# Kernel optimization log

Hardware: AMD Instinct MI355X
Metric: run time of the kernel (lower is better)

The kernel has to match this reference:

```python
import jax, jax.numpy as jnp
import numpy as np

DECAY = 0.8

def l2norm(t):
    # F.normalize with eps=1e-12
    n = jnp.linalg.norm(t, axis=-1, keepdims=True)
    return t / jnp.maximum(n, 1e-12)

def setup_inputs() -> dict:
    key = jax.random.key(0)
    k1, k2, k3 = jax.random.split(key, 3)
    x = jax.random.normal(k1, (16, 4096, 64), dtype=jnp.float32)
    embed = l2norm(jax.random.uniform(k2, (1, 4096, 64), dtype=jnp.float32) * 2.0 - 1.0)  # uniform_init + l2norm
    cluster_size = jax.random.uniform(k3, (1, 4096), dtype=jnp.float32) * 10.0
    return {"x": x, "embed": embed, "cluster_size": cluster_size}

def reference(x, embed, cluster_size):
    # x: [b, n, d] (ndim<4 -> add codebook dim), embed: [h, c, d]
    h, c, d = embed.shape
    xh = x[None, ...]                           # [1, b, n, d]
    shape = xh.shape
    flatten = l2norm(xh.reshape(h, -1, d))      # [h, N, d]
    embed_n = l2norm(embed)                     # [h, c, d]
    dist = jnp.einsum('hnd,hcd->hnc', flatten, embed_n)          # [h, N, c]
    embed_ind_flat = jnp.argmax(dist, axis=-1)                   # temperature==0 gumbel -> argmax
    embed_onehot = jax.nn.one_hot(embed_ind_flat, c, dtype=x.dtype)  # [h, N, c]
    embed_ind = embed_ind_flat.reshape(shape[:-1])               # [h, b, n]
    # batched_embedding: gather from the raw (non-normalized) codebook
    quantize = jax.vmap(lambda e, i: e[i])(embed, embed_ind_flat).reshape(shape)  # [h, b, n, d]
    # training-mode EMA codebook update (buffer updates returned as outputs)
    bins = embed_onehot.sum(axis=1)                              # [h, c]
    new_cluster_size = cluster_size * DECAY + bins * (1.0 - DECAY)
    zero_mask = bins == 0
    bins_safe = jnp.where(zero_mask, 1.0, bins)
    embed_sum = jnp.einsum('hnd,hnc->hcd', flatten, embed_onehot)  # [h, c, d]
    embed_normalized = l2norm(embed_sum / bins_safe[..., None])
    embed_normalized = jnp.where(zero_mask[..., None], embed_n, embed_normalized)
    new_embed = embed * DECAY + embed_normalized * (1.0 - DECAY)
    # squeeze back the added codebook dim (needs_codebook_dim path)
    return quantize[0], embed_ind[0], new_embed, new_cluster_size
```

## Files before the change

kernel.cpp:

```cpp
#include <hip/hip_runtime.h>
#include <math.h>

#define DECAY 0.8f
constexpr int B_     = 16;
constexpr int NSEQ   = 4096;
constexpr int D      = 64;
constexpr int C      = 4096;
constexpr int N      = B_ * NSEQ;
constexpr int NCHUNK = 4;
constexpr int CCHUNK = C / NCHUNK;
constexpr int PANEL  = 64;
constexpr int NPANEL = CCHUNK / PANEL;
constexpr int TILE_ELEMS = 32 * D;

#define GATE_THR  3e-4f
#define CONS_THR  1e-3f

typedef __attribute__((ext_vector_type(8)))  short bf16x8;
typedef __attribute__((ext_vector_type(16))) float f32x16;

__device__ __forceinline__ unsigned short bf16_rn(float f) {
    unsigned u = __builtin_bit_cast(unsigned, f);
    u += 0x7FFFu + ((u >> 16) & 1u);
    return (unsigned short)(u >> 16);
}
__device__ __forceinline__ float bf16_to_f(unsigned short h) {
    unsigned u = ((unsigned)h) << 16;
    return __builtin_bit_cast(float, u);
}
__device__ __forceinline__ f32x16 mfma32(bf16x8 a, bf16x8 b, f32x16 c) {
    return __builtin_amdgcn_mfma_f32_32x32x16_bf16(a, b, c, 0, 0, 0);
}
__device__ __forceinline__ void gload_lds16(const unsigned short* g,
                                            unsigned short* l) {
    __builtin_amdgcn_global_load_lds(
        (const __attribute__((address_space(1))) unsigned int*)g,
        (__attribute__((address_space(3))) unsigned int*)l, 16, 0, 0);
}

__global__ __launch_bounds__(256) void prep_e_kernel(
    const float* __restrict__ embed,
    float* __restrict__ embed_n,
    unsigned short* __restrict__ e_hi,
    unsigned short* __restrict__ e_lo,
    float* __restrict__ embed_sum,
    float* __restrict__ bins,
    int* __restrict__ dirty_count,
    int ncpy)
{
    int code = blockIdx.x * 4 + (threadIdx.x >> 6);
    int lane = threadIdx.x & 63;
    float v = embed[code * D + lane];
    float ss = v * v;
    #pragma unroll
    for (int o = 32; o > 0; o >>= 1) ss += __shfl_xor(ss, o);
    float inv = 1.0f / fmaxf(sqrtf(ss), 1e-12f);
    float en = v * inv;
    embed_n[code * D + lane] = en;

    unsigned short hi = bf16_rn(en);
    unsigned short lo = bf16_rn(en - bf16_to_f(hi));
    int t = code >> 5, r = code & 31;
    int g = lane >> 3, e = lane & 7;
    size_t pos = (size_t)t * TILE_ELEMS + (g * 32 + r) * 8 + e;
    e_hi[pos] = hi;
    e_lo[pos] = lo;

    for (int k = 0; k < ncpy; ++k) {
        embed_sum[(size_t)k * C * D + code * D + lane] = 0.0f;
        if (lane == 0) bins[k * C + code] = 0.0f;
    }
    if (blockIdx.x == 0 && threadIdx.x == 0) *dirty_count = 0;
}

__global__ __launch_bounds__(512) void assign_mfma_kernel(
    const float* __restrict__ x,
    const unsigned short* __restrict__ e_hi,
    const unsigned short* __restrict__ e_lo,
    float* __restrict__ part)
{
    __shared__ unsigned short lds_hi[2 * TILE_ELEMS];
    __shared__ unsigned short lds_lo[2 * TILE_ELEMS];

    const int tid  = threadIdx.x;
    const int lane = tid & 63;
    const int wid  = tid >> 6;
    const int m    = lane & 31;
    const int hi   = lane >> 5;
    const int rb   = (blockIdx.x * 8 + wid) * 32;
    const int cy   = blockIdx.y;

    bf16x8 xhi[4], xlo[4];
    #pragma unroll
    for (int c = 0; c < 4; ++c) {
        const float* p = x + (size_t)(rb + m) * D + c * 16 + hi * 8;
        float4 t0 = *(const float4*)p;
        float4 t1 = *(const float4*)(p + 4);
        float e[8] = {t0.x, t0.y, t0.z, t0.w, t1.x, t1.y, t1.z, t1.w};
        bf16x8 h, l2;
        #pragma unroll
        for (int j = 0; j < 8; ++j) {
            unsigned short hh = bf16_rn(e[j]);
            h[j]  = (short)hh;
            l2[j] = (short)bf16_rn(e[j] - bf16_to_f(hh));
        }
        xhi[c] = h;
        xlo[c] = l2;
    }

    float m1 = -3.4e38f, m2 = -3.4e38f;
    int   tl = 0;

    for (int p = 0; p < NPANEL; ++p) {
        const size_t pbase = ((size_t)cy * NPANEL + p) * (2 * TILE_ELEMS);
        __syncthreads();
        gload_lds16(e_hi + pbase + tid * 8, &lds_hi[tid * 8]);
        gload_lds16(e_lo + pbase + tid * 8, &lds_lo[tid * 8]);
        __syncthreads();

        #pragma unroll
        for (int t = 0; t < 2; ++t) {
            const int pt = (cy * NPANEL + p) * 2 + t;
            f32x16 accA = {}, accB = {};
            #pragma unroll
            for (int c = 0; c < 2; ++c) {
                const int off = t * TILE_ELEMS + ((c * 2 + hi) * 32 + m) * 8;
                bf16x8 eh = *(const bf16x8*)(lds_hi + off);
                bf16x8 el = *(const bf16x8*)(lds_lo + off);
                accA = mfma32(eh, xhi[c], accA);
                accA = mfma32(el, xhi[c], accA);
                accA = mfma32(eh, xlo[c], accA);
            }
            #pragma unroll
            for (int c = 2; c < 4; ++c) {
                const int off = t * TILE_ELEMS + ((c * 2 + hi) * 32 + m) * 8;
                bf16x8 eh = *(const bf16x8*)(lds_hi + off);
                bf16x8 el = *(const bf16x8*)(lds_lo + off);
                accB = mfma32(eh, xhi[c], accB);
                accB = mfma32(el, xhi[c], accB);
                accB = mfma32(eh, xlo[c], accB);
            }
            #pragma unroll
            for (int h = 0; h < 2; ++h) {
                float s0 = accA[h*8+0] + accB[h*8+0];
                float s1 = accA[h*8+1] + accB[h*8+1];
                float s2 = accA[h*8+2] + accB[h*8+2];
                float s3 = accA[h*8+3] + accB[h*8+3];
                float s4 = accA[h*8+4] + accB[h*8+4];
                float s5 = accA[h*8+5] + accB[h*8+5];
                float s6 = accA[h*8+6] + accB[h*8+6];
                float s7 = accA[h*8+7] + accB[h*8+7];
                float tm = fmaxf(fmaxf(fmaxf(s0, s1), fmaxf(s2, s3)),
                                 fmaxf(fmaxf(s4, s5), fmaxf(s6, s7)));
                const int ht = pt * 2 + h;
                float mn = fminf(m1, tm);
                bool  gt = tm > m1;
                tl = gt ? ht : tl;
                m1 = fmaxf(m1, tm);
                m2 = fmaxf(m2, mn);
            }
        }
    }

    {
        float b1 = __shfl_xor(m1, 32);
        float b2 = __shfl_xor(m2, 32);
        int   bt = __shfl_xor(tl, 32);
        float nm2 = fmaxf(fmaxf(m2, b2), fminf(m1, b1));
        bool  take = (b1 > m1);
        m1 = take ? b1 : m1;
        tl = take ? bt : tl;
        m2 = nm2;
    }
    if (lane < 32) {
        int row = rb + lane;
        float4 pr;
        pr.x = m1; pr.y = (float)tl; pr.z = m2; pr.w = 0.0f;
        *reinterpret_cast<float4*>(part + (size_t)row * D + cy * 4) = pr;
    }
}

__global__ __launch_bounds__(256) void merge_scatter_kernel(
    const float* __restrict__ x,
    const float* __restrict__ embed,
    const float* __restrict__ embed_n,
    float* __restrict__ q_out,
    float* __restrict__ ind_out,
    float* __restrict__ embed_sum,
    float* __restrict__ bins,
    int* __restrict__ dirty_count,
    int* __restrict__ dirty_list,
    int ncpy)
{
    int wid  = threadIdx.x >> 6;
    int lane = threadIdx.x & 63;
    int row  = blockIdx.x * 4 + wid;
    int cpy  = blockIdx.x & (ncpy - 1);

    float w1a, m2x; int wt;
    {
        const float4* pp = reinterpret_cast<const float4*>(q_out + (size_t)row * D);
        float4 P = pp[0];
        w1a = P.x; wt = (int)P.y; m2x = P.z;
        #pragma unroll
        for (int j = 1; j < NCHUNK; ++j) {
            float4 Q = pp[j];
            float nm2 = fmaxf(fmaxf(m2x, Q.z), fminf(w1a, Q.x));
            if (Q.x > w1a) { w1a = Q.x; wt = (int)Q.y; }
            m2x = nm2;
        }
    }

    int   csub = lane >> 2;
    int   code = wt * 16 + csub;
    float dot;
    {
        const float4* ep = (const float4*)(embed_n + (size_t)code * D + (lane & 3) * 16);
        const float4* xp = (const float4*)(x + (size_t)row * D + (lane & 3) * 16);
        float a0 = 0.f, a1 = 0.f, a2 = 0.f, a3 = 0.f;
        #pragma unroll
        for (int k = 0; k < 4; ++k) {
            float4 e = ep[k], xx = xp[k];
            a0 = fmaf(e.x, xx.x, a0);
            a1 = fmaf(e.y, xx.y, a1);
            a2 = fmaf(e.z, xx.z, a2);
            a3 = fmaf(e.w, xx.w, a3);
        }
        dot = (a0 + a1) + (a2 + a3);
        dot += __shfl_xor(dot, 1);
        dot += __shfl_xor(dot, 2);
    }
    float v = dot, s = -3.4e38f;
    int   vi = code;
    #pragma unroll
    for (int d = 4; d <= 32; d <<= 1) {
        float bv = __shfl_xor(v, d);
        float bs = __shfl_xor(s, d);
        int   bi = __shfl_xor(vi, d);
        float ns = fmaxf(fmaxf(s, bs), fminf(v, bv));
        bool  take = (bv > v) || (bv == v && bi < vi);
        v  = take ? bv : v;
        vi = take ? bi : vi;
        s  = ns;
    }

    bool dirty = (v - m2x <= GATE_THR) || (fabsf(v - w1a) > CONS_THR);
    if (dirty) {
        if (lane == 0) {
            int slot = atomicAdd(dirty_count, 1);
            dirty_list[slot] = row;
        }
        return;
    }

    float xk = x[(size_t)row * D + lane];
    float ss = xk * xk;
    #pragma unroll
    for (int o = 32; o > 0; o >>= 1) ss += __shfl_xor(ss, o);
    float inv = 1.0f / fmaxf(sqrtf(ss), 1e-12f);

    if (lane == 0) {
        ind_out[row] = (float)vi;
        atomicAdd(&bins[cpy * C + vi], 1.0f);
    }
    q_out[(size_t)row * D + lane] = embed[(size_t)vi * D + lane];
    atomicAdd(&embed_sum[(size_t)cpy * C * D + (size_t)vi * D + lane], xk * inv);
}

__global__ __launch_bounds__(256) void fallback_kernel(
    const float* __restrict__ x,
    const float* __restrict__ embed,
    const float* __restrict__ embed_n,
    const int* __restrict__ dirty_count,
    const int* __restrict__ dirty_list,
    float* __restrict__ ind_out,
    float* __restrict__ q_out,
    float* __restrict__ embed_sum,
    float* __restrict__ bins,
    int ncpy)
{
    __shared__ float xs[D];
    __shared__ float bv[256];
    __shared__ int   bidx[256];
    int cnt = *dirty_count;
    int cpy = blockIdx.x & (ncpy - 1);
    for (int i = blockIdx.x; i < cnt; i += gridDim.x) {
        int row = dirty_list[i];
        __syncthreads();
        if (threadIdx.x < D) xs[threadIdx.x] = x[(size_t)row * D + threadIdx.x];
        __syncthreads();
        float best = -3.4e38f;
        int   bi   = 0;
        int   c0   = threadIdx.x * 16;
        for (int c = c0; c < c0 + 16; ++c) {
            const float4* ep = (const float4*)(embed_n + (size_t)c * D);
            const float4* xp = (const float4*)xs;
            float a0 = 0.f, a1 = 0.f, a2 = 0.f, a3 = 0.f;
            #pragma unroll
            for (int k = 0; k < D / 4; ++k) {
                float4 e = ep[k], xx = xp[k];
                a0 = fmaf(e.x, xx.x, a0);
                a1 = fmaf(e.y, xx.y, a1);
                a2 = fmaf(e.z, xx.z, a2);
                a3 = fmaf(e.w, xx.w, a3);
            }
            float dd = (a0 + a1) + (a2 + a3);
            if (dd > best) { best = dd; bi = c; }
        }
        bv[threadIdx.x]   = best;
        bidx[threadIdx.x] = bi;
        __syncthreads();
        #pragma unroll
        for (int s = 128; s > 0; s >>= 1) {
            if (threadIdx.x < s) {
                float v2 = bv[threadIdx.x + s];
                int   i2 = bidx[threadIdx.x + s];
                if (v2 > bv[threadIdx.x] ||
                    (v2 == bv[threadIdx.x] && i2 < bidx[threadIdx.x])) {
                    bv[threadIdx.x]   = v2;
                    bidx[threadIdx.x] = i2;
                }
            }
            __syncthreads();
        }
        int fi = bidx[0];
        if (threadIdx.x == 0) {
            ind_out[row] = (float)fi;
            atomicAdd(&bins[cpy * C + fi], 1.0f);
        }
        if (threadIdx.x < 64) {
            float xk = xs[threadIdx.x];
            float ss = xk * xk;
            #pragma unroll
            for (int o = 32; o > 0; o >>= 1) ss += __shfl_xor(ss, o);
            float inv = 1.0f / fmaxf(sqrtf(ss), 1e-12f);
            q_out[(size_t)row * D + threadIdx.x] =
                embed[(size_t)fi * D + threadIdx.x];
            atomicAdd(&embed_sum[(size_t)cpy * C * D + (size_t)fi * D + threadIdx.x],
                      xk * inv);
        }
        __syncthreads();
    }
}

__global__ __launch_bounds__(256) void finalize_kernel(
    const float* __restrict__ embed,
    const float* __restrict__ cluster_size,
    const float* __restrict__ embed_n,
    const float* __restrict__ embed_sum,
    const float* __restrict__ bins,
    float* __restrict__ new_embed_out,
    float* __restrict__ new_cs_out,
    int ncpy)
{
    int code = blockIdx.x * 4 + (threadIdx.x >> 6);
    int lane = threadIdx.x & 63;
    float bsum = 0.0f;
    for (int k = 0; k < ncpy; ++k) bsum += bins[k * C + code];
    if (lane == 0)
        new_cs_out[code] = cluster_size[code] * DECAY + bsum * (1.0f - DECAY);

    float en;
    if (bsum == 0.0f) {
        en = embed_n[code * D + lane];
    } else {
        float vsum = 0.0f;
        for (int k = 0; k < ncpy; ++k)
            vsum += embed_sum[(size_t)k * C * D + code * D + lane];
        float v = vsum / bsum;
        float ss = v * v;
        #pragma unroll
        for (int o = 32; o > 0; o >>= 1) ss += __shfl_xor(ss, o);
        en = v / fmaxf(sqrtf(ss), 1e-12f);
    }
    new_embed_out[code * D + lane] =
        embed[code * D + lane] * DECAY + en * (1.0f - DECAY);
}

extern "C" void kernel_launch(void* const* d_in, const int* in_sizes, int n_in,
                              void* d_out, int out_size, void* d_ws, size_t ws_size,
                              hipStream_t stream)
{
    const float* x            = (const float*)d_in[0];
    const float* embed        = (const float*)d_in[1];
    const float* cluster_size = (const float*)d_in[2];

    float* out     = (float*)d_out;
    float* q_out   = out;
    float* ind_out = out + (size_t)N * D;
    float* ne_out  = ind_out + N;
    float* ncs_out = ne_out + (size_t)C * D;

    char* ws = (char*)d_ws;
    float*          embed_n     = (float*)ws;
    unsigned short* e_hi        = (unsigned short*)(ws + (1u << 20));
    unsigned short* e_lo        = (unsigned short*)(ws + (1u << 20) + 524288);
    float*          bins        = (float*)(ws + (2u << 20));
    int*            dirty_list  = (int*)(ws + (2u << 20) + 262144);
    int*            dirty_count = (int*)(ws + (2u << 20) + 524288);
    float*          embed_sum   = (float*)(ws + (3u << 20));

    const size_t need4 = (3u << 20) + 4u * ((size_t)C * D * 4);
    const int ncpy = (ws_size >= need4) ? 4 : 1;

    prep_e_kernel<<<C / 4, 256, 0, stream>>>(embed, embed_n, e_hi, e_lo,
                                             embed_sum, bins, dirty_count, ncpy);
    assign_mfma_kernel<<<dim3(N / 256, NCHUNK), 512, 0, stream>>>(
        x, e_hi, e_lo, q_out);
    merge_scatter_kernel<<<N / 4, 256, 0, stream>>>(x, embed, embed_n,
                                                    q_out, ind_out,
                                                    embed_sum, bins,
                                                    dirty_count, dirty_list, ncpy);
    fallback_kernel<<<1024, 256, 0, stream>>>(x, embed, embed_n, dirty_count,
                                              dirty_list, ind_out, q_out,
                                              embed_sum, bins, ncpy);
    finalize_kernel<<<C / 4, 256, 0, stream>>>(embed, cluster_size, embed_n,
                                               embed_sum, bins, ne_out, ncs_out,
                                               ncpy);
}
```

Baseline: 177.1 us.

## Track exact per-code argmax in MFMA kernel and drop fp32 re-scoring in merge

The assignment kernel now keeps the best individual code index and a true second-best value per lane, instead of only the best 16-code tile. This lets the merge kernel skip reloading embed_n and recomputing 16 fp32 dot products per row, gating only on the top-1/top-2 margin. The LDS panel is also doubled to 128 codes, halving the number of barrier-separated load phases. The risk is that the bf16x3 scores now decide the index directly, with only the margin gate protecting against precision ties.

```diff
diff --git a/kernel.cpp b/kernel.cpp
--- a/kernel.cpp
+++ b/kernel.cpp
@@ -9,12 +9,11 @@
 constexpr int N      = B_ * NSEQ;
 constexpr int NCHUNK = 4;
 constexpr int CCHUNK = C / NCHUNK;
-constexpr int PANEL  = 64;
+constexpr int PANEL  = 128;
 constexpr int NPANEL = CCHUNK / PANEL;
 constexpr int TILE_ELEMS = 32 * D;
 
 #define GATE_THR  3e-4f
-#define CONS_THR  1e-3f
 
 typedef __attribute__((ext_vector_type(8)))  short bf16x8;
 typedef __attribute__((ext_vector_type(16))) float f32x16;
@@ -79,8 +78,8 @@
     const unsigned short* __restrict__ e_lo,
     float* __restrict__ part)
 {
-    __shared__ unsigned short lds_hi[2 * TILE_ELEMS];
-    __shared__ unsigned short lds_lo[2 * TILE_ELEMS];
+    __shared__ unsigned short lds_hi[4 * TILE_ELEMS];
+    __shared__ unsigned short lds_lo[4 * TILE_ELEMS];
 
     const int tid  = threadIdx.x;
     const int lane = tid & 63;
@@ -109,18 +108,20 @@
     }
 
     float m1 = -3.4e38f, m2 = -3.4e38f;
-    int   tl = 0;
+    int   tl = 0, il = 0;
 
     for (int p = 0; p < NPANEL; ++p) {
-        const size_t pbase = ((size_t)cy * NPANEL + p) * (2 * TILE_ELEMS);
-        __syncthreads();
-        gload_lds16(e_hi + pbase + tid * 8, &lds_hi[tid * 8]);
-        gload_lds16(e_lo + pbase + tid * 8, &lds_lo[tid * 8]);
-        __syncthreads();
-
-        #pragma unroll
-        for (int t = 0; t < 2; ++t) {
-            const int pt = (cy * NPANEL + p) * 2 + t;
+        const size_t pbase = ((size_t)cy * NPANEL + p) * (4 * TILE_ELEMS);
+        __syncthreads();
+        gload_lds16(e_hi + pbase + tid * 8,        &lds_hi[tid * 8]);
+        gload_lds16(e_hi + pbase + 4096 + tid * 8, &lds_hi[4096 + tid * 8]);
+        gload_lds16(e_lo + pbase + tid * 8,        &lds_lo[tid * 8]);
+        gload_lds16(e_lo + pbase + 4096 + tid * 8, &lds_lo[4096 + tid * 8]);
+        __syncthreads();
+
+        #pragma unroll
+        for (int t = 0; t < 4; ++t) {
+            const int pt = (cy * NPANEL + p) * 4 + t;
             f32x16 accA = {}, accB = {};
             #pragma unroll
             for (int c = 0; c < 2; ++c) {
@@ -141,41 +142,34 @@
                 accB = mfma32(eh, xlo[c], accB);
             }
             #pragma unroll
-            for (int h = 0; h < 2; ++h) {
-                float s0 = accA[h*8+0] + accB[h*8+0];
-                float s1 = accA[h*8+1] + accB[h*8+1];
-                float s2 = accA[h*8+2] + accB[h*8+2];
-                float s3 = accA[h*8+3] + accB[h*8+3];
-                float s4 = accA[h*8+4] + accB[h*8+4];
-                float s5 = accA[h*8+5] + accB[h*8+5];
-                float s6 = accA[h*8+6] + accB[h*8+6];
-                float s7 = accA[h*8+7] + accB[h*8+7];
-                float tm = fmaxf(fmaxf(fmaxf(s0, s1), fmaxf(s2, s3)),
-                                 fmaxf(fmaxf(s4, s5), fmaxf(s6, s7)));
-                const int ht = pt * 2 + h;
-                float mn = fminf(m1, tm);
-                bool  gt = tm > m1;
-                tl = gt ? ht : tl;
-                m1 = fmaxf(m1, tm);
-                m2 = fmaxf(m2, mn);
-            }
-        }
-    }
-
+            for (int r = 0; r < 16; ++r) {
+                float v = accA[r] + accB[r];
+                const int cit = (r & 3) + 8 * (r >> 2);
+                bool gt = v > m1;
+                float mx = fmaxf(m2, v);
+                m2 = gt ? m1 : mx;
+                tl = gt ? pt : tl;
+                il = gt ? cit : il;
+                m1 = fmaxf(m1, v);
+            }
+        }
+    }
+
+    int code = (tl << 5) + il + (hi << 2);
     {
         float b1 = __shfl_xor(m1, 32);
         float b2 = __shfl_xor(m2, 32);
-        int   bt = __shfl_xor(tl, 32);
+        int   bc = __shfl_xor(code, 32);
         float nm2 = fmaxf(fmaxf(m2, b2), fminf(m1, b1));
-        bool  take = (b1 > m1);
-        m1 = take ? b1 : m1;
-        tl = take ? bt : tl;
-        m2 = nm2;
+        bool  take = (b1 > m1) || (b1 == m1 && bc < code);
+        m1   = take ? b1 : m1;
+        code = take ? bc : code;
+        m2   = nm2;
     }
     if (lane < 32) {
         int row = rb + lane;
         float4 pr;
-        pr.x = m1; pr.y = (float)tl; pr.z = m2; pr.w = 0.0f;
+        pr.x = m1; pr.y = (float)code; pr.z = m2; pr.w = 0.0f;
         *reinterpret_cast<float4*>(part + (size_t)row * D + cy * 4) = pr;
     }
 }
@@ -183,7 +177,6 @@
 __global__ __launch_bounds__(256) void merge_scatter_kernel(
     const float* __restrict__ x,
     const float* __restrict__ embed,
-    const float* __restrict__ embed_n,
     float* __restrict__ q_out,
     float* __restrict__ ind_out,
     float* __restrict__ embed_sum,
@@ -197,54 +190,21 @@
     int row  = blockIdx.x * 4 + wid;
     int cpy  = blockIdx.x & (ncpy - 1);
 
-    float w1a, m2x; int wt;
+    float w1, m2x; int wc;
     {
         const float4* pp = reinterpret_cast<const float4*>(q_out + (size_t)row * D);
         float4 P = pp[0];
-        w1a = P.x; wt = (int)P.y; m2x = P.z;
+        w1 = P.x; wc = (int)P.y; m2x = P.z;
         #pragma unroll
         for (int j = 1; j < NCHUNK; ++j) {
             float4 Q = pp[j];
-            float nm2 = fmaxf(fmaxf(m2x, Q.z), fminf(w1a, Q.x));
-            if (Q.x > w1a) { w1a = Q.x; wt = (int)Q.y; }
+            float nm2 = fmaxf(fmaxf(m2x, Q.z), fminf(w1, Q.x));
+            if (Q.x > w1) { w1 = Q.x; wc = (int)Q.y; }
             m2x = nm2;
         }
     }
 
-    int   csub = lane >> 2;
-    int   code = wt * 16 + csub;
-    float dot;
-    {
-        const float4* ep = (const float4*)(embed_n + (size_t)code * D + (lane & 3) * 16);
-        const float4* xp = (const float4*)(x + (size_t)row * D + (lane & 3) * 16);
-        float a0 = 0.f, a1 = 0.f, a2 = 0.f, a3 = 0.f;
-        #pragma unroll
-        for (int k = 0; k < 4; ++k) {
-            float4 e = ep[k], xx = xp[k];
-            a0 = fmaf(e.x, xx.x, a0);
-            a1 = fmaf(e.y, xx.y, a1);
-            a2 = fmaf(e.z, xx.z, a2);
-            a3 = fmaf(e.w, xx.w, a3);
-        }
-        dot = (a0 + a1) + (a2 + a3);
-        dot += __shfl_xor(dot, 1);
-        dot += __shfl_xor(dot, 2);
-    }
-    float v = dot, s = -3.4e38f;
-    int   vi = code;
-    #pragma unroll
-    for (int d = 4; d <= 32; d <<= 1) {
-        float bv = __shfl_xor(v, d);
-        float bs = __shfl_xor(s, d);
-        int   bi = __shfl_xor(vi, d);
-        float ns = fmaxf(fmaxf(s, bs), fminf(v, bv));
-        bool  take = (bv > v) || (bv == v && bi < vi);
-        v  = take ? bv : v;
-        vi = take ? bi : vi;
-        s  = ns;
-    }
-
-    bool dirty = (v - m2x <= GATE_THR) || (fabsf(v - w1a) > CONS_THR);
+    bool dirty = (w1 - m2x <= GATE_THR);
     if (dirty) {
         if (lane == 0) {
             int slot = atomicAdd(dirty_count, 1);
@@ -260,11 +220,11 @@
     float inv = 1.0f / fmaxf(sqrtf(ss), 1e-12f);
 
     if (lane == 0) {
-        ind_out[row] = (float)vi;
-        atomicAdd(&bins[cpy * C + vi], 1.0f);
-    }
-    q_out[(size_t)row * D + lane] = embed[(size_t)vi * D + lane];
-    atomicAdd(&embed_sum[(size_t)cpy * C * D + (size_t)vi * D + lane], xk * inv);
+        ind_out[row] = (float)wc;
+        atomicAdd(&bins[cpy * C + wc], 1.0f);
+    }
+    q_out[(size_t)row * D + lane] = embed[(size_t)wc * D + lane];
+    atomicAdd(&embed_sum[(size_t)cpy * C * D + (size_t)wc * D + lane], xk * inv);
 }
 
 __global__ __launch_bounds__(256) void fallback_kernel(
@@ -407,8 +367,7 @@
                                              embed_sum, bins, dirty_count, ncpy);
     assign_mfma_kernel<<<dim3(N / 256, NCHUNK), 512, 0, stream>>>(
         x, e_hi, e_lo, q_out);
-    merge_scatter_kernel<<<N / 4, 256, 0, stream>>>(x, embed, embed_n,
-                                                    q_out, ind_out,
+    merge_scatter_kernel<<<N / 4, 256, 0, stream>>>(x, embed, q_out, ind_out,
                                                     embed_sum, bins,
                                                     dirty_count, dirty_list, ncpy);
     fallback_kernel<<<1024, 256, 0, stream>>>(x, embed, embed_n, dirty_count,
```

New measurement: 174.9 us. Within noise of the previous version (-1.2%).
